# Kernel optimization log

Measured on AMD Instinct MI355X. Metric: run time of the kernel, lower is better.

The kernel has to match this reference:

```python
import jax, jax.numpy as jnp
import numpy as np
from jax import lax

RATIOS = (0.5, 1.0, 2.0)
SCALES = (8, 16, 32)
STRIDE = 16
N_ANCHOR = 9
N_PRE = 6000      # eval-mode n_pre_nms
N_POST = 300      # eval-mode n_post_nms
NMS_THRESH = 0.7
MIN_SIZE = 16.0


def _anchor_base():
    rows = []
    for r in RATIOS:
        for s in SCALES:
            h = STRIDE * s * np.sqrt(r)
            w = STRIDE * s * np.sqrt(1.0 / r)
            c = STRIDE / 2.0
            rows.append([c - h / 2.0, c - w / 2.0, c + h / 2.0, c + w / 2.0])
    return jnp.asarray(np.array(rows, np.float32))  # [9,4]


def _all_anchors(hh, ww):
    ab = _anchor_base()
    sy, sx = jnp.meshgrid(jnp.arange(hh) * STRIDE, jnp.arange(ww) * STRIDE, indexing='ij')
    shift = jnp.stack([sy.ravel(), sx.ravel(), sy.ravel(), sx.ravel()], axis=1).astype(jnp.float32)
    return (shift[:, None, :] + ab[None, :, :]).reshape(-1, 4)  # [hh*ww*9, 4]


def _conv(x, w, b, pad):
    y = lax.conv_general_dilated(x, w, (1, 1), ((pad, pad), (pad, pad)),
                                 dimension_numbers=('NCHW', 'OIHW', 'NCHW'))
    return y + b[None, :, None, None]


def _loc2bbox(anchor, loc):
    ah = anchor[:, 2] - anchor[:, 0]
    aw = anchor[:, 3] - anchor[:, 1]
    acy = anchor[:, 0] + 0.5 * ah
    acx = anchor[:, 1] + 0.5 * aw
    dy, dx, dh, dw = loc[:, 0], loc[:, 1], loc[:, 2], loc[:, 3]
    cy = dy * ah + acy
    cx = dx * aw + acx
    h = jnp.exp(dh) * ah
    w = jnp.exp(dw) * aw
    return jnp.stack([cy - 0.5 * h, cx - 0.5 * w, cy + 0.5 * h, cx + 0.5 * w], axis=1)


def _iou_matrix(boxes):
    tl = jnp.maximum(boxes[:, None, :2], boxes[None, :, :2])
    br = jnp.minimum(boxes[:, None, 2:], boxes[None, :, 2:])
    wh = jnp.clip(br - tl, 0.0)
    inter = wh[..., 0] * wh[..., 1]
    area = (boxes[:, 2] - boxes[:, 0]) * (boxes[:, 3] - boxes[:, 1])
    return inter / (area[:, None] + area[None, :] - inter + 1e-9)


def _nms_keep(boxes, valid):
    # boxes sorted by descending score; sequential greedy NMS via fori_loop.
    iou = _iou_matrix(boxes)
    idx = jnp.arange(boxes.shape[0])

    def body(i, keep):
        sup = keep[i] & (iou[i] > NMS_THRESH) & (idx > i)
        return keep & ~sup

    return lax.fori_loop(0, boxes.shape[0], body, valid)


def _proposals(loc, fg_score, anchors, img_h, img_w):
    boxes = _loc2bbox(anchors, loc)
    boxes = jnp.clip(boxes, 0.0, jnp.array([img_h, img_w, img_h, img_w], jnp.float32))
    hs = boxes[:, 2] - boxes[:, 0]
    ws = boxes[:, 3] - boxes[:, 1]
    valid = (hs >= MIN_SIZE) & (ws >= MIN_SIZE)
    score = jnp.where(valid, fg_score, -jnp.inf)
    topv, topi = lax.top_k(score, N_PRE)          # pre-NMS selection by score
    boxes = boxes[topi]
    keep = _nms_keep(boxes, topv > -jnp.inf)
    # compact first N_POST kept boxes (score order), zero-padded if fewer.
    rank = jnp.cumsum(keep) - 1
    pos = jnp.where(keep & (rank < N_POST), rank, N_POST)
    return jnp.zeros((N_POST + 1, 4), boxes.dtype).at[pos].set(boxes)[:N_POST]


def setup_inputs():
    key = jax.random.key(0)
    ks = jax.random.split(key, 4)
    C = 512
    return {
        'feature_map': jax.random.normal(ks[0], (2, C, 64, 64), jnp.float32),
        'conv1_w': jax.random.normal(ks[1], (C, C, 3, 3), jnp.float32) * 0.01,
        'conv1_b': jnp.zeros((C,), jnp.float32),
        'score_w': jax.random.normal(ks[2], (N_ANCHOR * 2, C, 1, 1), jnp.float32) * 0.01,
        'score_b': jnp.zeros((N_ANCHOR * 2,), jnp.float32),
        'loc_w': jax.random.normal(ks[3], (N_ANCHOR * 4, C, 1, 1), jnp.float32) * 0.01,
        'loc_b': jnp.zeros((N_ANCHOR * 4,), jnp.float32),
        'img_h': 1024,
        'img_w': 1024,
    }


def reference(feature_map, conv1_w, conv1_b, score_w, score_b, loc_w, loc_b, img_h, img_w):
    n, _, hh, ww = feature_map.shape
    h = jax.nn.relu(_conv(feature_map, conv1_w, conv1_b, 1))
    rpn_locs = _conv(h, loc_w, loc_b, 0).transpose(0, 2, 3, 1).reshape(n, -1, 4)
    scores_raw = _conv(h, score_w, score_b, 0).transpose(0, 2, 3, 1)  # [n,hh,ww,18]
    sm = jax.nn.softmax(scores_raw.reshape(n, hh, ww, N_ANCHOR, 2), axis=4)
    rpn_fg_scores = sm[..., 1].reshape(n, -1)
    rpn_scores = scores_raw.reshape(n, -1, 2)
    anchors = _all_anchors(hh, ww)
    rois = jax.vmap(lambda l, s: _proposals(l, s, anchors, img_h, img_w))(rpn_locs, rpn_fg_scores)
    roi_indices = jnp.repeat(jnp.arange(n, dtype=jnp.int32), N_POST)
    return rpn_locs, rpn_scores, rois.reshape(-1, 4), roi_indices, anchors
```

## Files before the change

kernel.cpp:

```cpp
#include <hip/hip_runtime.h>
#include <cmath>

#define NANCH 36864
#define NPRE 6000
#define NPOST 300

#define LOCS_OFF   0
#define SCORES_OFF 294912
#define ROIS_OFF   442368
#define RIDX_OFF   444768
#define ANCH_OFF   445368

#define WT_OFF      0ull
#define WTH_OFF     0ull
#define WTL_OFF     4718592ull
#define PREFIX_OFF  2097152ull
#define PREFIXM_OFF 2621440ull
#define SORTED_OFF  3145728ull
#define MASK_OFF    0ull
#define H_OFF       9437184ull
#define BOXES_OFF   26214400ull
#define W54_OFF     26214400ull
#define KEYS_OFF    27394048ull
#define HIST_OFF    27983872ull
#define SKEYS_OFF   28631168ull
#define SBOXES_OFF  28727168ull
#define VMASK_OFF   29033856ull
#define XTH_OFF     29360128ull
#define XTL_OFF     37748736ull
#define WS_NEED_MFMA 46137344ull

typedef _Float16 half8 __attribute__((ext_vector_type(8)));
typedef float floatx4 __attribute__((ext_vector_type(4)));

__device__ __forceinline__ void load_lds16(const float* g, float* l) {
#if __has_builtin(__builtin_amdgcn_global_load_lds)
  __builtin_amdgcn_global_load_lds(
      (const __attribute__((address_space(1))) void*)g,
      (__attribute__((address_space(3))) void*)l, 16, 0, 0);
#else
  int lane = threadIdx.x & 63;
  float4 v = *(const float4*)g;
  *(float4*)((char*)l + lane * 16) = v;
#endif
}

__device__ __forceinline__ void load_lds16g(const void* g, void* l) {
#if __has_builtin(__builtin_amdgcn_global_load_lds)
  __builtin_amdgcn_global_load_lds(
      (const __attribute__((address_space(1))) void*)g,
      (__attribute__((address_space(3))) void*)l, 16, 0, 0);
#else
  int lane = threadIdx.x & 63;
  float4 v = *(const float4*)g;
  *(float4*)((char*)l + lane * 16) = v;
#endif
}

__global__ __launch_bounds__(1024) void prep_kernel(
    const float* __restrict__ w, float* __restrict__ wt,
    const float* __restrict__ lw, const float* __restrict__ sw,
    float* __restrict__ w54p) {
  __shared__ float lds[9][32][33];
  if (blockIdx.x < 256) {
    int tx = threadIdx.x & 31;
    int ty = threadIdx.x >> 5;
    int ci0 = (blockIdx.x & 15) * 32;
    int co0 = (blockIdx.x >> 4) * 32;
    const float* src = w + ((size_t)(co0 + ty) * 512 + (ci0 + tx)) * 9;
#pragma unroll
    for (int k = 0; k < 9; k++) lds[k][tx][ty] = src[k];
    __syncthreads();
#pragma unroll
    for (int k = 0; k < 9; k++) {
      wt[((size_t)k * 512 + (ci0 + ty)) * 512 + co0 + tx] = lds[k][ty][tx];
    }
  } else {
    int t = (blockIdx.x - 256) * 1024 + threadIdx.x;
    int k = t >> 6, co = t & 63;
    float v = 0.f;
    if (co < 36) v = lw[(size_t)co * 512 + k];
    else if (co < 54) v = sw[(size_t)(co - 36) * 512 + k];
    w54p[t] = v;
  }
}

__global__ __launch_bounds__(1024) void prep16_kernel(
    const float* __restrict__ w, _Float16* __restrict__ wth,
    _Float16* __restrict__ wtl, const float* __restrict__ lw,
    const float* __restrict__ sw, float* __restrict__ w54p) {
  if (blockIdx.x < 256) {
    int tx = threadIdx.x & 31;
    int ty = threadIdx.x >> 5;
    int ci0 = (blockIdx.x & 15) * 32;
    int co0 = (blockIdx.x >> 4) * 32;
    int ci = ci0 + tx, co = co0 + ty;
    const float* src = w + ((size_t)co * 512 + ci) * 9;
    int cot = co >> 7, coin = co & 127;
    int cs = ci >> 5, gg = (ci >> 3) & 3, cii = ci & 7;
    size_t obase = ((((size_t)cot) * 16 + cs) * 4 + gg) * 1024 +
                   (size_t)coin * 8 + cii;
#pragma unroll
    for (int k = 0; k < 9; k++) {
      float v = src[k];
      _Float16 h = (_Float16)v;
      _Float16 l = (_Float16)((v - (float)h) * 1024.f);
      size_t o = (size_t)k * 262144 + obase;
      wth[o] = h;
      wtl[o] = l;
    }
  } else {
    int t = (blockIdx.x - 256) * 1024 + threadIdx.x;
    int k = t >> 6, co = t & 63;
    float v = 0.f;
    if (co < 36) v = lw[(size_t)co * 512 + k];
    else if (co < 54) v = sw[(size_t)(co - 36) * 512 + k];
    w54p[t] = v;
  }
}

__global__ __launch_bounds__(256) void prepx_kernel(
    const float* __restrict__ x, _Float16* __restrict__ xth,
    _Float16* __restrict__ xtl) {
  __shared__ float xs[32][65];
  int b = blockIdx.x;
  int cs = b & 15, ny = b >> 4;
  int n = ny >> 6, y = ny & 63;
  int tid = threadIdx.x;
  const float* xb = x + ((size_t)n << 21) + (y << 6);
#pragma unroll
  for (int p = 0; p < 8; p++) {
    int c = p * 4 + (tid >> 6);
    xs[c][tid & 63] = xb[((size_t)(cs * 32 + c) << 12) + (tid & 63)];
  }
  __syncthreads();
  int px = tid & 63, gx = tid >> 6;
  unsigned int hw[4], lw2[4];
#pragma unroll
  for (int j = 0; j < 4; j++) {
    float v0 = xs[gx * 8 + 2 * j][px], v1 = xs[gx * 8 + 2 * j + 1][px];
    _Float16 h0 = (_Float16)v0, h1 = (_Float16)v1;
    _Float16 l0 = (_Float16)((v0 - (float)h0) * 1024.f);
    _Float16 l1 = (_Float16)((v1 - (float)h1) * 1024.f);
    hw[j] = (unsigned int)__builtin_bit_cast(unsigned short, h0) |
            ((unsigned int)__builtin_bit_cast(unsigned short, h1) << 16);
    lw2[j] = (unsigned int)__builtin_bit_cast(unsigned short, l0) |
             ((unsigned int)__builtin_bit_cast(unsigned short, l1) << 16);
  }
  size_t o = (size_t)b * 2048 + (size_t)gx * 512 + (size_t)px * 8;
  uint4 hv; hv.x = hw[0]; hv.y = hw[1]; hv.z = hw[2]; hv.w = hw[3];
  uint4 lv; lv.x = lw2[0]; lv.y = lw2[1]; lv.z = lw2[2]; lv.w = lw2[3];
  *(uint4*)(xth + o) = hv;
  *(uint4*)(xtl + o) = lv;
}

__global__ __launch_bounds__(256, 3) void conv1_mfma_kernel(
    const _Float16* __restrict__ xth, const _Float16* __restrict__ xtl,
    const _Float16* __restrict__ wth, const _Float16* __restrict__ wtl,
    const float* __restrict__ bias, float* __restrict__ hout) {
  __shared__ __align__(16) _Float16 sXh[6336];
  __shared__ __align__(16) _Float16 sXl[6336];
  __shared__ __align__(16) _Float16 sWh[4096];
  __shared__ __align__(16) _Float16 sWl[4096];
  int mb = blockIdx.x;
  int n = mb >> 6, y = mb & 63;
  int co0 = blockIdx.y << 7;
  int tid = threadIdx.x;
  int wv = tid >> 6, lane = tid & 63;
  int m15 = lane & 15, g = lane >> 4;

  floatx4 accm[2][4], accl[2][4];
#pragma unroll
  for (int ct = 0; ct < 2; ct++)
#pragma unroll
    for (int pt = 0; pt < 4; pt++) {
      accm[ct][pt] = (floatx4){0.f, 0.f, 0.f, 0.f};
      accl[ct][pt] = (floatx4){0.f, 0.f, 0.f, 0.f};
    }

  for (int t2 = tid; t2 < 3168; t2 += 256) {
    ((unsigned int*)sXh)[t2] = 0u;
    ((unsigned int*)sXl)[t2] = 0u;
  }
  __syncthreads();

  bool yv0 = (y > 0), yv2 = (y < 63);
  int p = wv >> 1, hf = wv & 1;
  _Float16* wdst = p ? sWl : sWh;
  const _Float16* wsel = p ? wtl : wth;

  for (int cs = 0; cs < 16; cs++) {
    {
      int base = wv * 6;
#pragma unroll
      for (int i = 0; i < 6; i++) {
        int idx = base + i;
        int yr = idx >> 3, rem = idx & 7;
        int part = rem >> 2, d = rem & 3;
        int ys = y + yr - 1;
        if (ys >= 0 && ys < 64) {
          const _Float16* s =
              (part ? xtl : xth) +
              ((((size_t)(n * 64 + ys)) * 16 + cs) << 11) + (d << 9) +
              (lane << 3);
          _Float16* dst = (part ? sXl : sXh) + yr * 2112 + d * 528 + 8;
          load_lds16g(s, dst);
        }
      }
    }
    size_t woff0 = (size_t)(co0 >> 7) * 65536 + (size_t)cs * 4096;
    const _Float16* wsrc0 = wsel + woff0 + (lane << 3);
#pragma unroll
    for (int tap = 0; tap < 9; tap++) {
      int ky = tap / 3;
      int kx = tap - ky * 3;
      if (ky == 0 && !yv0) continue;
      if (ky == 2 && !yv2) continue;
      const _Float16* ws = wsrc0 + (size_t)tap * 262144;
#pragma unroll
      for (int e = 0; e < 4; e++) {
        int gd = hf * 2 + (e >> 1), half = e & 1;
        load_lds16g(ws + gd * 1024 + half * 512,
                    wdst + gd * 1024 + half * 512);
      }
      __syncthreads();
      half8 Ah[2], Al[2], Bh[4], Bl[4];
#pragma unroll
      for (int ct = 0; ct < 2; ct++) {
        int ao = (g << 10) + (((wv << 5) + (ct << 4) + m15) << 3);
        Ah[ct] = *(const half8*)(sWh + ao);
        Al[ct] = *(const half8*)(sWl + ao);
      }
#pragma unroll
      for (int pt = 0; pt < 4; pt++) {
        int bo = ky * 2112 + g * 528 + (((pt << 4) + m15 + kx) << 3);
        Bh[pt] = *(const half8*)(sXh + bo);
        Bl[pt] = *(const half8*)(sXl + bo);
      }
#pragma unroll
      for (int ct = 0; ct < 2; ct++)
#pragma unroll
        for (int pt = 0; pt < 4; pt++) {
          accm[ct][pt] = __builtin_amdgcn_mfma_f32_16x16x32_f16(
              Ah[ct], Bh[pt], accm[ct][pt], 0, 0, 0);
          accl[ct][pt] = __builtin_amdgcn_mfma_f32_16x16x32_f16(
              Ah[ct], Bl[pt], accl[ct][pt], 0, 0, 0);
          accl[ct][pt] = __builtin_amdgcn_mfma_f32_16x16x32_f16(
              Al[ct], Bh[pt], accl[ct][pt], 0, 0, 0);
        }
      __syncthreads();
    }
  }

#pragma unroll
  for (int ct = 0; ct < 2; ct++)
#pragma unroll
    for (int pt = 0; pt < 4; pt++) {
#pragma unroll
      for (int r = 0; r < 4; r++) {
        int co = co0 + (wv << 5) + (ct << 4) + (g << 2) + r;
        float v = accm[ct][pt][r] + accl[ct][pt][r] * 0.0009765625f +
                  bias[co];
        hout[((size_t)(n * 512 + co) << 12) + (y << 6) + (pt << 4) + m15] =
            fmaxf(v, 0.f);
      }
    }
}

__global__ __launch_bounds__(256) void conv1_kernel(
    const float* __restrict__ x, const float* __restrict__ wt,
    const float* __restrict__ bias, float* __restrict__ hout) {
  __shared__ __align__(16) float smem[10752];
  int mb = blockIdx.x;
  int n = mb >> 6, y = mb & 63;
  int co0 = blockIdx.y << 7;
  int tid = threadIdx.x;
  int team = tid >> 7;
  int tl = tid & 127;
  int cibase = team << 8;
  float* Asb = smem + team * 768;
  float* Bsb = smem + 1536 + team * 4608;
  int tx = tl & 7, ty = tl >> 3;
  int x0 = tx << 3;

  float acc[8][8];
#pragma unroll
  for (int j = 0; j < 8; j++)
#pragma unroll
    for (int i = 0; i < 8; i++) acc[j][i] = 0.f;

  const float* xb = x + ((size_t)n << 21);

  if (y == 0) {
    for (int t2 = tl; t2 < 256; t2 += 128) Asb[t2] = 0.f;
  }
  if (y == 63) {
    for (int t2 = tl; t2 < 256; t2 += 128) Asb[512 + t2] = 0.f;
  }

  int wv = tl >> 6;
  int lane = tl & 63;
  int lrow = lane >> 5;
  int lcol = (lane & 31) << 2;
  int aci = lane >> 4;
  int aoff = (lane & 15) << 2;

  for (int cc = 0; cc < 256; cc += 4) {
    int ci0 = cibase + cc;
    for (int yr = wv; yr < 3; yr += 2) {
      int ys = y + yr - 1;
      if (ys >= 0 && ys < 64) {
        const float* g =
            xb + (((size_t)(ci0 + aci)) << 12) + (ys << 6) + aoff;
        load_lds16(g, &Asb[yr << 8]);
      }
    }
    for (int i = 0; i < 9; i++) {
      int r0 = i * 4 + wv * 2;
      int row = r0 + lrow;
      int kk = row >> 2, ci = row & 3;
      const float* g = wt + (((size_t)(kk << 9)) + ci0 + ci) * 512 + co0 + lcol;
      load_lds16(g, &Bsb[r0 << 7]);
    }
    __syncthreads();
    for (int k = 0; k < 4; k++) {
#pragma unroll
      for (int ky = 0; ky < 3; ky++) {
        const float* arr = &Asb[((ky << 2) + k) << 6];
        float w10[10];
        w10[0] = (tx == 0) ? 0.f : arr[x0 - 1];
        float4 a0 = *(const float4*)&arr[x0];
        float4 a1 = *(const float4*)&arr[x0 + 4];
        w10[1] = a0.x; w10[2] = a0.y; w10[3] = a0.z; w10[4] = a0.w;
        w10[5] = a1.x; w10[6] = a1.y; w10[7] = a1.z; w10[8] = a1.w;
        w10[9] = (tx == 7) ? 0.f : arr[x0 + 8];
#pragma unroll
        for (int kx = 0; kx < 3; kx++) {
          int kk = ky * 3 + kx;
          const float* br = &Bsb[(((kk << 2) + k) << 7) + (ty << 3)];
          float4 b0 = *(const float4*)br;
          float4 b1 = *(const float4*)(br + 4);
          float bb[8] = {b0.x, b0.y, b0.z, b0.w, b1.x, b1.y, b1.z, b1.w};
#pragma unroll
          for (int j = 0; j < 8; j++)
#pragma unroll
            for (int dx = 0; dx < 8; dx++)
              acc[j][dx] = fmaf(w10[kx + dx], bb[j], acc[j][dx]);
        }
      }
    }
    __syncthreads();
  }

  if (team == 1) {
#pragma unroll
    for (int j = 0; j < 8; j++) {
      *(float4*)&smem[tl * 68 + (j << 3)] = *(float4*)&acc[j][0];
      *(float4*)&smem[tl * 68 + (j << 3) + 4] = *(float4*)&acc[j][4];
    }
  }
  __syncthreads();
  if (team == 0) {
#pragma unroll
    for (int j = 0; j < 8; j++) {
      int co = co0 + (ty << 3) + j;
      float bv = bias[co];
      float4 p0 = *(float4*)&smem[tl * 68 + (j << 3)];
      float4 p1 = *(float4*)&smem[tl * 68 + (j << 3) + 4];
      float4 v0, v1;
      v0.x = fmaxf((acc[j][0] + p0.x) + bv, 0.f);
      v0.y = fmaxf((acc[j][1] + p0.y) + bv, 0.f);
      v0.z = fmaxf((acc[j][2] + p0.z) + bv, 0.f);
      v0.w = fmaxf((acc[j][3] + p0.w) + bv, 0.f);
      v1.x = fmaxf((acc[j][4] + p1.x) + bv, 0.f);
      v1.y = fmaxf((acc[j][5] + p1.y) + bv, 0.f);
      v1.z = fmaxf((acc[j][6] + p1.z) + bv, 0.f);
      v1.w = fmaxf((acc[j][7] + p1.w) + bv, 0.f);
      float* o = &hout[(((size_t)(n * 512 + co)) << 12) + (y << 6) + x0];
      *(float4*)o = v0;
      *(float4*)(o + 4) = v1;
    }
  }
}

__global__ __launch_bounds__(256) void heads_kernel(
    const float* __restrict__ h, const float* __restrict__ w54p,
    const float* __restrict__ loc_b, const float* __restrict__ score_b,
    float* __restrict__ out) {
  __shared__ __align__(16) float hs[32 * 64];
  __shared__ __align__(16) float wsd[32 * 64];
  __shared__ float sacc[64 * 65];
  int n = blockIdx.x >> 6;
  int p0 = (blockIdx.x & 63) << 6;
  int tid = threadIdx.x;
  int txp = tid & 63;
  int tw = tid >> 6;
  float acc[16];
#pragma unroll
  for (int j = 0; j < 16; j++) acc[j] = 0.f;
  const float* hb = h + ((size_t)n * 512) * 4096 + p0;
  for (int k0 = 0; k0 < 512; k0 += 32) {
    for (int t = tid; t < 512; t += 256) {
      int r = t >> 4, l = (t & 15) << 2;
      *(float4*)&hs[(r << 6) + l] =
          *(const float4*)&hb[(((size_t)(k0 + r)) << 12) + l];
      *(float4*)&wsd[(r << 6) + l] =
          *(const float4*)&w54p[((k0 + r) << 6) + l];
    }
    __syncthreads();
    for (int k = 0; k < 32; k++) {
      float hv = hs[(k << 6) + txp];
      const float* wr = &wsd[(k << 6) + (tw << 4)];
#pragma unroll
      for (int u = 0; u < 4; u++) {
        float4 wv = *(const float4*)(wr + (u << 2));
        acc[u * 4 + 0] = fmaf(hv, wv.x, acc[u * 4 + 0]);
        acc[u * 4 + 1] = fmaf(hv, wv.y, acc[u * 4 + 1]);
        acc[u * 4 + 2] = fmaf(hv, wv.z, acc[u * 4 + 2]);
        acc[u * 4 + 3] = fmaf(hv, wv.w, acc[u * 4 + 3]);
      }
    }
    __syncthreads();
  }
#pragma unroll
  for (int j = 0; j < 16; j++) sacc[(tw * 16 + j) * 65 + txp] = acc[j];
  __syncthreads();
  for (int t = tid; t < 64 * 54; t += 256) {
    int p = t / 54, c = t - p * 54;
    float v = sacc[c * 65 + p];
    int gp = (n << 12) + p0 + p;
    if (c < 36) out[LOCS_OFF + (size_t)gp * 36 + c] = v + loc_b[c];
    else out[SCORES_OFF + (size_t)gp * 18 + (c - 36)] = v + score_b[c - 36];
  }
}

__global__ void decode_kernel(const float* __restrict__ out_ro,
                              const int* __restrict__ pimh,
                              const int* __restrict__ pimw,
                              float* __restrict__ boxes,
                              unsigned long long* __restrict__ keys,
                              unsigned int* __restrict__ hist,
                              float* __restrict__ out) {
  int t = blockIdx.x * 256 + threadIdx.x;
  int n = t / NANCH, k = t - n * NANCH;
  float imh = (float)pimh[0], imw = (float)pimw[0];

  int a = k % 9, pos = k / 9;
  int jj = pos & 63, ii = pos >> 6;
  int ridx = a / 3, sidx = a % 3;
  double r = (ridx == 0) ? 0.5 : ((ridx == 1) ? 1.0 : 2.0);
  double s = (sidx == 0) ? 8.0 : ((sidx == 1) ? 16.0 : 32.0);
  double ahh = 16.0 * s * sqrt(r);
  double aww = 16.0 * s * sqrt(1.0 / r);
  float b0 = (float)(8.0 - ahh / 2.0), b1 = (float)(8.0 - aww / 2.0);
  float b2 = (float)(8.0 + ahh / 2.0), b3 = (float)(8.0 + aww / 2.0);
  float sy = (float)(ii * 16), sx = (float)(jj * 16);
  float a0 = sy + b0, a1 = sx + b1, a2 = sy + b2, a3 = sx + b3;
  if (n == 0) {
    float* o = out + ANCH_OFF + (size_t)k * 4;
    o[0] = a0; o[1] = a1; o[2] = a2; o[3] = a3;
  }

  const float* loc = out_ro + LOCS_OFF + (size_t)t * 4;
  const float* sc = out_ro + SCORES_OFF + (size_t)t * 2;
  float ah = __fsub_rn(a2, a0), aw = __fsub_rn(a3, a1);
  float acy = __fadd_rn(a0, 0.5f * ah), acx = __fadd_rn(a1, 0.5f * aw);
  float dy = loc[0], dx = loc[1], dh = loc[2], dw = loc[3];
  float cy = __fadd_rn(__fmul_rn(dy, ah), acy);
  float cx = __fadd_rn(__fmul_rn(dx, aw), acx);
  float hh = __fmul_rn(expf(dh), ah);
  float ww = __fmul_rn(expf(dw), aw);
  float y1 = __fsub_rn(cy, 0.5f * hh), x1 = __fsub_rn(cx, 0.5f * ww);
  float y2 = __fadd_rn(cy, 0.5f * hh), x2 = __fadd_rn(cx, 0.5f * ww);
  y1 = fminf(fmaxf(y1, 0.f), imh); x1 = fminf(fmaxf(x1, 0.f), imw);
  y2 = fminf(fmaxf(y2, 0.f), imh); x2 = fminf(fmaxf(x2, 0.f), imw);
  bool valid = (__fsub_rn(y2, y1) >= 16.f) && (__fsub_rn(x2, x1) >= 16.f);
  float s0 = sc[0], s1 = sc[1];
  float m = fmaxf(s0, s1);
  float e0 = expf(__fsub_rn(s0, m)), e1 = expf(__fsub_rn(s1, m));
  float fg = __fdiv_rn(e1, __fadd_rn(e0, e1));
  float score = valid ? fg : -INFINITY;
  unsigned int u = __float_as_uint(score);
  unsigned int ord = (u & 0x80000000u) ? ~u : (u | 0x80000000u);
  unsigned long long key =
      ((unsigned long long)(~ord) << 16) | (unsigned long long)(k & 0xFFFF);
  float4 b4; b4.x = y1; b4.y = x1; b4.z = y2; b4.w = x2;
  *(float4*)(boxes + (size_t)t * 4) = b4;
  keys[t] = key;
  if (valid)
    atomicAdd(&hist[((size_t)n << 16) + (unsigned int)(key >> 32)], 1u);
}

__global__ __launch_bounds__(1024) void scanfull_kernel(
    const unsigned int* __restrict__ hist, unsigned int* __restrict__ prefix,
    unsigned int* __restrict__ prefix_mut) {
  int n = blockIdx.x;
  const uint4* h4 = (const uint4*)(hist + ((size_t)n << 16));
  uint4* pf4 = (uint4*)(prefix + ((size_t)n << 16));
  uint4* pm4 = (uint4*)(prefix_mut + ((size_t)n << 16));
  __shared__ unsigned int ps[1024];
  int tid = threadIdx.x;
  int base4 = tid << 4;
  uint4 vals[16];
  unsigned int s = 0;
#pragma unroll
  for (int i = 0; i < 16; i++) {
    vals[i] = h4[base4 + i];
    s += vals[i].x + vals[i].y + vals[i].z + vals[i].w;
  }
  ps[tid] = s;
  __syncthreads();
  for (int off = 1; off < 1024; off <<= 1) {
    unsigned int v = ps[tid];
    unsigned int add = (tid >= off) ? ps[tid - off] : 0u;
    __syncthreads();
    ps[tid] = v + add;
    __syncthreads();
  }
  unsigned int run = ps[tid] - s;
#pragma unroll
  for (int i = 0; i < 16; i++) {
    uint4 hv = vals[i];
    uint4 pv;
    pv.x = run; run += hv.x;
    pv.y = run; run += hv.y;
    pv.z = run; run += hv.z;
    pv.w = run; run += hv.w;
    pf4[base4 + i] = pv;
    pm4[base4 + i] = pv;
  }
}

__global__ void scatter_kernel(const unsigned long long* __restrict__ keys,
                               unsigned int* __restrict__ prefix_mut,
                               unsigned long long* __restrict__ sorted) {
  int t = blockIdx.x * 256 + threadIdx.x;
  int n = t / NANCH;
  unsigned long long key = keys[t];
  unsigned int b = (unsigned int)(key >> 32);
  if (b >= 0xFF80u) return;
  unsigned int pos = atomicAdd(&prefix_mut[((size_t)n << 16) + b], 1u);
  if (pos < 8192) sorted[((size_t)n << 13) + pos] = key;
}

__global__ void fixup_kernel(const unsigned long long* __restrict__ sorted,
                             const unsigned int* __restrict__ prefix,
                             const unsigned int* __restrict__ hist,
                             const float* __restrict__ boxes,
                             unsigned long long* __restrict__ skeys,
                             float* __restrict__ sboxes) {
  int t = blockIdx.x * 256 + threadIdx.x;
  int n = t / 7168;
  int s = t - n * 7168;
  const unsigned long long* srt = sorted + ((size_t)n << 13);
  unsigned long long key = srt[s];
  unsigned int hi = (unsigned int)(key >> 16);
  if (hi >= 0xFF800000u) {
    if (s < NPRE) skeys[(size_t)n * NPRE + s] = key;
    return;
  }
  unsigned int b = (unsigned int)(key >> 32);
  unsigned int st = prefix[((size_t)n << 16) + b];
  if (st >= (unsigned)NPRE) return;
  unsigned int cnt = hist[((size_t)n << 16) + b];
  unsigned int r = 0;
  if (cnt > 1) {
    for (unsigned int j = 0; j < cnt; j++) r += (srt[st + j] < key) ? 1u : 0u;
  }
  unsigned int pos = st + r;
  if (pos < (unsigned)NPRE) {
    skeys[(size_t)n * NPRE + pos] = key;
    int k = (int)(key & 0xFFFFull);
    float4 bx = *(const float4*)(boxes + (((size_t)n * NANCH) + k) * 4);
    *(float4*)(sboxes + ((size_t)n * NPRE + pos) * 4) = bx;
  }
}

__global__ __launch_bounds__(64) void nms_mask_kernel(
    const float* __restrict__ sboxes,
    const unsigned long long* __restrict__ skeys,
    unsigned long long* __restrict__ vmask,
    unsigned long long* __restrict__ mask) {
  int n = blockIdx.z;
  int ib = blockIdx.x, jb = blockIdx.y;
  if (jb < ib) return;
  int lane = threadIdx.x;
  __shared__ __align__(16) float jbox[64][4];
  int j = jb * 64 + lane;
  float4 bj4 = (j < NPRE)
                   ? *(const float4*)(sboxes + ((size_t)n * NPRE + j) * 4)
                   : float4{0.f, 0.f, 0.f, 0.f};
  *(float4*)jbox[lane] = bj4;
  __syncthreads();
  if (jb == ib) {
    int idx = ib * 64 + lane;
    bool ok = false;
    if (idx < NPRE) {
      unsigned int khi = (unsigned int)(skeys[(size_t)n * NPRE + idx] >> 16);
      ok = khi < 0xFF800000u;
    }
    unsigned long long m = __ballot(ok);
    if (lane == 0) vmask[(size_t)n * 94 + ib] = m;
  }
  int i = ib * 64 + lane;
  if (i >= NPRE) return;
  float4 bi = *(const float4*)(sboxes + ((size_t)n * NPRE + i) * 4);
  float ay1 = bi.x, ax1 = bi.y, ay2 = bi.z, ax2 = bi.w;
  float areaA = __fmul_rn(__fsub_rn(ay2, ay1), __fsub_rn(ax2, ax1));
  unsigned long long bits = 0ull;
#pragma unroll 8
  for (int l = 0; l < 64; l++) {
    float4 bj = *(const float4*)jbox[l];
    float ty1 = fmaxf(ay1, bj.x), tx1 = fmaxf(ax1, bj.y);
    float ty2 = fminf(ay2, bj.z), tx2 = fminf(ax2, bj.w);
    float wh0 = fmaxf(__fsub_rn(ty2, ty1), 0.f);
    float wh1 = fmaxf(__fsub_rn(tx2, tx1), 0.f);
    float inter = __fmul_rn(wh0, wh1);
    float areaB = __fmul_rn(__fsub_rn(bj.z, bj.x), __fsub_rn(bj.w, bj.y));
    float den = __fadd_rn(__fsub_rn(__fadd_rn(areaA, areaB), inter), 1e-9f);
    float iou = __fdiv_rn(inter, den);
    if (iou > 0.7f) bits |= (1ull << l);
  }
  mask[((size_t)n * NPRE + i) * 94 + jb] = bits;
}

#define WARM_ROWS 2048

__global__ __launch_bounds__(1024) void nms_reduce_kernel(
    const unsigned long long* __restrict__ mask,
    const unsigned long long* __restrict__ vmask,
    const float* __restrict__ sboxes, float* __restrict__ out) {
  int n = blockIdx.x;
  __shared__ int kept[NPOST];

  {
    const ulonglong2* m2 =
        (const ulonglong2*)(mask + (size_t)n * NPRE * 94);
    unsigned long long accw = 0;
    const int total = WARM_ROWS * 94 / 2;
    for (int i = threadIdx.x; i < total; i += 1024) {
      ulonglong2 v = m2[i];
      accw ^= v.x ^ v.y;
    }
    asm volatile("" :: "v"(accw));
  }
  __syncthreads();
  if (threadIdx.x >= 64) return;

  int lane = threadIdx.x;

  unsigned long long rlo = ~vmask[(size_t)n * 94 + lane];
  unsigned long long rhi = (64 + lane < 94) ? ~vmask[(size_t)n * 94 + 64 + lane]
                                            : ~0ull;
  int count = 0;
  for (int c = 0; c < 94 && count < NPOST; c++) {
    unsigned long long curw =
        (c < 64) ? __shfl(rlo, c) : __shfl(rhi, c - 64);
    unsigned long long cand = ~curw;
    while (cand != 0ull && count < NPOST) {
      int b = __builtin_ctzll(cand);
      int i = c * 64 + b;
      if (lane == 0) kept[count] = i;
      count++;
      const unsigned long long* row = mask + ((size_t)n * NPRE + i) * 94;
      unsigned long long r0 = row[lane];
      unsigned long long r1 = (64 + lane < 94) ? row[64 + lane] : 0ull;
      rlo |= r0; rhi |= r1;
      curw = (c < 64) ? __shfl(rlo, c) : __shfl(rhi, c - 64);
      cand = ~curw;
      cand &= (b == 63) ? 0ull : (~0ull << (b + 1));
    }
  }

  float* rois = out + ROIS_OFF + (size_t)n * NPOST * 4;
  float* ridx = out + RIDX_OFF + (size_t)n * NPOST;
  for (int s = lane; s < NPOST; s += 64) {
    float4 v = {0.f, 0.f, 0.f, 0.f};
    if (s < count) {
      int i = kept[s];
      v = *(const float4*)(sboxes + ((size_t)n * NPRE + i) * 4);
    }
    *(float4*)(rois + (size_t)s * 4) = v;
    ridx[s] = (float)n;
  }
}

extern "C" void kernel_launch(void* const* d_in, const int* in_sizes, int n_in,
                              void* d_out, int out_size, void* d_ws,
                              size_t ws_size, hipStream_t stream) {
  const float* feat = (const float*)d_in[0];
  const float* w1 = (const float*)d_in[1];
  const float* b1 = (const float*)d_in[2];
  const float* sw = (const float*)d_in[3];
  const float* sb = (const float*)d_in[4];
  const float* lw = (const float*)d_in[5];
  const float* lb = (const float*)d_in[6];
  const int* pimh = (const int*)d_in[7];
  const int* pimw = (const int*)d_in[8];
  float* out = (float*)d_out;
  char* ws = (char*)d_ws;

  float* wt = (float*)(ws + WT_OFF);
  _Float16* wth = (_Float16*)(ws + WTH_OFF);
  _Float16* wtl = (_Float16*)(ws + WTL_OFF);
  _Float16* xth = (_Float16*)(ws + XTH_OFF);
  _Float16* xtl = (_Float16*)(ws + XTL_OFF);
  float* w54p = (float*)(ws + W54_OFF);
  float* hbuf = (float*)(ws + H_OFF);
  float* boxes = (float*)(ws + BOXES_OFF);
  unsigned long long* keys = (unsigned long long*)(ws + KEYS_OFF);
  unsigned int* hist = (unsigned int*)(ws + HIST_OFF);
  unsigned int* prefix = (unsigned int*)(ws + PREFIX_OFF);
  unsigned int* prefix_mut = (unsigned int*)(ws + PREFIXM_OFF);
  unsigned long long* sorted = (unsigned long long*)(ws + SORTED_OFF);
  unsigned long long* skeys = (unsigned long long*)(ws + SKEYS_OFF);
  float* sboxes = (float*)(ws + SBOXES_OFF);
  unsigned long long* vmask = (unsigned long long*)(ws + VMASK_OFF);
  unsigned long long* nmask = (unsigned long long*)(ws + MASK_OFF);

  hipMemsetAsync(ws + HIST_OFF, 0, 524288, stream);
  hipMemsetAsync(ws + SORTED_OFF, 0xFF, 131072, stream);

  bool big = (ws_size >= WS_NEED_MFMA);
  if (big) {
    prep16_kernel<<<288, 1024, 0, stream>>>(w1, wth, wtl, lw, sw, w54p);
    prepx_kernel<<<2048, 256, 0, stream>>>(feat, xth, xtl);
    conv1_mfma_kernel<<<dim3(128, 4), 256, 0, stream>>>(xth, xtl, wth, wtl,
                                                        b1, hbuf);
  } else {
    prep_kernel<<<288, 1024, 0, stream>>>(w1, wt, lw, sw, w54p);
    conv1_kernel<<<dim3(128, 4), 256, 0, stream>>>(feat, wt, b1, hbuf);
  }
  heads_kernel<<<128, 256, 0, stream>>>(hbuf, w54p, lb, sb, out);
  decode_kernel<<<288, 256, 0, stream>>>(out, pimh, pimw, boxes, keys, hist,
                                         out);
  scanfull_kernel<<<2, 1024, 0, stream>>>(hist, prefix, prefix_mut);
  scatter_kernel<<<288, 256, 0, stream>>>(keys, prefix_mut, sorted);
  fixup_kernel<<<56, 256, 0, stream>>>(sorted, prefix, hist, boxes, skeys,
                                       sboxes);
  nms_mask_kernel<<<dim3(94, 94, 2), 64, 0, stream>>>(sboxes, skeys, vmask,
                                                      nmask);
  nms_reduce_kernel<<<2, 1024, 0, stream>>>(nmask, vmask, sboxes, out);
}
```

Before: 611.5 us.

## Load conv1 weights directly from global into registers, drop per-tap LDS staging

The conv1 MFMA kernel no longer stages each tap's weight tile through shared memory. Each wave now reads its A fragments straight from global memory into registers. This removes two barriers per tap, leaving two per channel slice, and frees 16 KB of LDS per block, which may allow more blocks per CU. The trade-off is that weight loads now go through global memory and cache with no cross-wave sharing, and their latency is exposed just before the MFMAs.

```diff
diff --git a/kernel.cpp b/kernel.cpp
--- a/kernel.cpp
+++ b/kernel.cpp
@@ -160,8 +160,6 @@
     const float* __restrict__ bias, float* __restrict__ hout) {
   __shared__ __align__(16) _Float16 sXh[6336];
   __shared__ __align__(16) _Float16 sXl[6336];
-  __shared__ __align__(16) _Float16 sWh[4096];
-  __shared__ __align__(16) _Float16 sWl[4096];
   int mb = blockIdx.x;
   int n = mb >> 6, y = mb & 63;
   int co0 = blockIdx.y << 7;
@@ -185,11 +183,11 @@
   __syncthreads();
 
   bool yv0 = (y > 0), yv2 = (y < 63);
-  int p = wv >> 1, hf = wv & 1;
-  _Float16* wdst = p ? sWl : sWh;
-  const _Float16* wsel = p ? wtl : wth;
+  size_t wlanebase = (size_t)(co0 >> 7) * 65536 + (size_t)g * 1024 +
+                     (size_t)(((wv << 5) + m15) << 3);
 
   for (int cs = 0; cs < 16; cs++) {
+    if (cs) __syncthreads();
     {
       int base = wv * 6;
 #pragma unroll
@@ -208,47 +206,41 @@
         }
       }
     }
-    size_t woff0 = (size_t)(co0 >> 7) * 65536 + (size_t)cs * 4096;
-    const _Float16* wsrc0 = wsel + woff0 + (lane << 3);
-#pragma unroll
-    for (int tap = 0; tap < 9; tap++) {
-      int ky = tap / 3;
-      int kx = tap - ky * 3;
+    __syncthreads();
+
+    const _Float16* whp = wth + wlanebase + (size_t)cs * 4096;
+    const _Float16* wlp = wtl + wlanebase + (size_t)cs * 4096;
+#pragma unroll
+    for (int ky = 0; ky < 3; ky++) {
       if (ky == 0 && !yv0) continue;
       if (ky == 2 && !yv2) continue;
-      const _Float16* ws = wsrc0 + (size_t)tap * 262144;
-#pragma unroll
-      for (int e = 0; e < 4; e++) {
-        int gd = hf * 2 + (e >> 1), half = e & 1;
-        load_lds16g(ws + gd * 1024 + half * 512,
-                    wdst + gd * 1024 + half * 512);
+#pragma unroll
+      for (int kx = 0; kx < 3; kx++) {
+        int tap = ky * 3 + kx;
+        size_t to = (size_t)tap * 262144;
+        half8 Ah[2], Al[2], Bh[4], Bl[4];
+        Ah[0] = *(const half8*)(whp + to);
+        Ah[1] = *(const half8*)(whp + to + 128);
+        Al[0] = *(const half8*)(wlp + to);
+        Al[1] = *(const half8*)(wlp + to + 128);
+#pragma unroll
+        for (int pt = 0; pt < 4; pt++) {
+          int bo = ky * 2112 + g * 528 + (((pt << 4) + m15 + kx) << 3);
+          Bh[pt] = *(const half8*)(sXh + bo);
+          Bl[pt] = *(const half8*)(sXl + bo);
+        }
+#pragma unroll
+        for (int ct = 0; ct < 2; ct++)
+#pragma unroll
+          for (int pt = 0; pt < 4; pt++) {
+            accm[ct][pt] = __builtin_amdgcn_mfma_f32_16x16x32_f16(
+                Ah[ct], Bh[pt], accm[ct][pt], 0, 0, 0);
+            accl[ct][pt] = __builtin_amdgcn_mfma_f32_16x16x32_f16(
+                Ah[ct], Bl[pt], accl[ct][pt], 0, 0, 0);
+            accl[ct][pt] = __builtin_amdgcn_mfma_f32_16x16x32_f16(
+                Al[ct], Bh[pt], accl[ct][pt], 0, 0, 0);
+          }
       }
-      __syncthreads();
-      half8 Ah[2], Al[2], Bh[4], Bl[4];
-#pragma unroll
-      for (int ct = 0; ct < 2; ct++) {
-        int ao = (g << 10) + (((wv << 5) + (ct << 4) + m15) << 3);
-        Ah[ct] = *(const half8*)(sWh + ao);
-        Al[ct] = *(const half8*)(sWl + ao);
-      }
-#pragma unroll
-      for (int pt = 0; pt < 4; pt++) {
-        int bo = ky * 2112 + g * 528 + (((pt << 4) + m15 + kx) << 3);
-        Bh[pt] = *(const half8*)(sXh + bo);
-        Bl[pt] = *(const half8*)(sXl + bo);
-      }
-#pragma unroll
-      for (int ct = 0; ct < 2; ct++)
-#pragma unroll
-        for (int pt = 0; pt < 4; pt++) {
-          accm[ct][pt] = __builtin_amdgcn_mfma_f32_16x16x32_f16(
-              Ah[ct], Bh[pt], accm[ct][pt], 0, 0, 0);
-          accl[ct][pt] = __builtin_amdgcn_mfma_f32_16x16x32_f16(
-              Ah[ct], Bl[pt], accl[ct][pt], 0, 0, 0);
-          accl[ct][pt] = __builtin_amdgcn_mfma_f32_16x16x32_f16(
-              Al[ct], Bh[pt], accl[ct][pt], 0, 0, 0);
-        }
-      __syncthreads();
     }
   }
 
```

Result: no change. 621.4 us (+1.6%).
